# Optimization experiments

Measured on AMD Instinct MI355X. Metric: run time of the kernel, lower is better.

Reference implementation:

```python
import jax, jax.numpy as jnp
import numpy as np

EMB = 1024
HEADS = 16
HD = EMB // HEADS
EPS = 1e-5

def _ln(x, g, b):
    m = jnp.mean(x, axis=-1, keepdims=True)
    v = jnp.mean((x - m) ** 2, axis=-1, keepdims=True)
    return (x - m) * jax.lax.rsqrt(v + EPS) * g + b

def setup_inputs() -> dict:
    key = jax.random.key(0)
    ks = jax.random.split(key, 12)
    s_in = 1.0 / np.sqrt(EMB)
    s_ff = 1.0 / np.sqrt(4 * EMB)
    return {
        "x": jax.random.normal(ks[0], (2, 2048, EMB), jnp.float32),
        "wq": jax.random.uniform(ks[1], (HEADS, EMB, HD), jnp.float32, -s_in, s_in),
        "wk": jax.random.uniform(ks[2], (HEADS, EMB, HD), jnp.float32, -s_in, s_in),
        "wv": jax.random.uniform(ks[3], (HEADS, EMB, HD), jnp.float32, -s_in, s_in),
        "wo": jax.random.uniform(ks[4], (EMB, EMB), jnp.float32, -s_in, s_in),
        "bo": jax.random.uniform(ks[5], (EMB,), jnp.float32, -s_in, s_in),
        "g1": jnp.ones((EMB,), jnp.float32),
        "b1": jnp.zeros((EMB,), jnp.float32),
        "g2": jnp.ones((EMB,), jnp.float32),
        "b2": jnp.zeros((EMB,), jnp.float32),
        "w1": jax.random.uniform(ks[6], (EMB, 4 * EMB), jnp.float32, -s_in, s_in),
        "bf1": jax.random.uniform(ks[7], (4 * EMB,), jnp.float32, -s_in, s_in),
        "w2": jax.random.uniform(ks[8], (4 * EMB, EMB), jnp.float32, -s_ff, s_ff),
        "bf2": jax.random.uniform(ks[9], (EMB,), jnp.float32, -s_ff, s_ff),
    }

def reference(x, wq, wk, wv, wo, bo, g1, b1, g2, b2, w1, bf1, w2, bf2):
    B, T, C = x.shape
    h = _ln(x, g1, b1)
    # all heads batched: [B,H,T,HD]
    q = jnp.einsum('btc,hcd->bhtd', h, wq)
    k = jnp.einsum('btc,hcd->bhtd', h, wk)
    v = jnp.einsum('btc,hcd->bhtd', h, wv)
    # NOTE: original scales by full emb_size C**-0.5, not head_size
    scores = jnp.einsum('bhtd,bhsd->bhts', q, k) * (C ** -0.5)
    causal = jnp.tril(jnp.ones((T, T), bool))
    scores = jnp.where(causal, scores, -jnp.inf)
    w = jax.nn.softmax(scores, axis=-1)
    attn = jnp.einsum('bhts,bhsd->bhtd', w, v)
    attn = attn.transpose(0, 2, 1, 3).reshape(B, T, C)  # concat heads
    x = x + attn @ wo + bo
    h2 = _ln(x, g2, b2)
    ffn = jax.nn.relu(h2 @ w1 + bf1) @ w2 + bf2
    return x + ffn
```

## Files before the change

kernel.cpp:

```cpp
#include <hip/hip_runtime.h>
#include <hip/hip_bf16.h>

typedef __bf16 bf16x8 __attribute__((ext_vector_type(8)));
typedef float f32x4 __attribute__((ext_vector_type(4)));
typedef short s16x8 __attribute__((ext_vector_type(8)));

#define DEV __device__ __forceinline__

DEV float b2f(unsigned short u) {
  unsigned int x = ((unsigned int)u) << 16;
  return __builtin_bit_cast(float, x);
}
DEV unsigned short f2b(float f) {
  unsigned int x = __builtin_bit_cast(unsigned int, f);
  x += 0x7fffu + ((x >> 16) & 1u);
  return (unsigned short)(x >> 16);
}
DEV unsigned int f2b2(float a, float b) {
  float2 t; t.x = a; t.y = b;
  __hip_bfloat162 v = __float22bfloat162_rn(t);
  unsigned int r;
  __builtin_memcpy(&r, &v, 4);
  return r;
}
DEV f32x4 mfma16(bf16x8 a, bf16x8 b, f32x4 c) {
  return __builtin_amdgcn_mfma_f32_16x16x32_bf16(a, b, c, 0, 0, 0);
}
DEV void gl2lds16(const unsigned short* g, unsigned short* l) {
  __builtin_amdgcn_global_load_lds(
      (const __attribute__((address_space(1))) void*)g,
      (__attribute__((address_space(3))) void*)l, 16, 0, 0);
}

__global__ __launch_bounds__(256)
void transpose_k(const float* __restrict__ in, unsigned short* __restrict__ out,
                 int K, int N, long zin, long zout) {
  __shared__ float tile[32][33];
  in  += (size_t)blockIdx.z * zin;
  out += (size_t)blockIdx.z * zout;
  int n0 = blockIdx.x * 32, k0 = blockIdx.y * 32;
  int tx = threadIdx.x, ty = threadIdx.y;
  #pragma unroll
  for (int i = ty; i < 32; i += 8)
    tile[i][tx] = in[(size_t)(k0 + i) * N + n0 + tx];
  __syncthreads();
  #pragma unroll
  for (int i = ty; i < 32; i += 8)
    out[(size_t)(n0 + i) * K + k0 + tx] = f2b(tile[tx][i]);
}

__global__ __launch_bounds__(256)
void transpose_qkv(const float* __restrict__ wq, const float* __restrict__ wk,
                   const float* __restrict__ wv, unsigned short* __restrict__ out) {
  __shared__ float tile[32][33];
  const int z = blockIdx.z;
  const float* in = (z < 16) ? (wq + (size_t)z * 65536)
                  : (z < 32) ? (wk + (size_t)(z - 16) * 65536)
                             : (wv + (size_t)(z - 32) * 65536);
  unsigned short* o = out + (size_t)z * 65536;
  int n0 = blockIdx.x * 32, k0 = blockIdx.y * 32;
  int tx = threadIdx.x, ty = threadIdx.y;
  #pragma unroll
  for (int i = ty; i < 32; i += 8)
    tile[i][tx] = in[(size_t)(k0 + i) * 64 + n0 + tx];
  __syncthreads();
  #pragma unroll
  for (int i = ty; i < 32; i += 8)
    o[(size_t)(n0 + i) * 1024 + k0 + tx] = f2b(tile[tx][i]);
}

__global__ __launch_bounds__(256)
void ln_kernel(const float* __restrict__ x, const float* __restrict__ g,
               const float* __restrict__ b, unsigned short* __restrict__ o) {
  __shared__ float rs[4];
  __shared__ float rq[4];
  int row = blockIdx.x, tid = threadIdx.x;
  const float* xr = x + (size_t)row * 1024;
  float4 raw = ((const float4*)xr)[tid];
  float s = raw.x + raw.y + raw.z + raw.w;
  float q = raw.x*raw.x + raw.y*raw.y + raw.z*raw.z + raw.w*raw.w;
  #pragma unroll
  for (int off = 32; off > 0; off >>= 1) {
    s += __shfl_down(s, off);
    q += __shfl_down(q, off);
  }
  int wave = tid >> 6;
  if ((tid & 63) == 0) { rs[wave] = s; rq[wave] = q; }
  __syncthreads();
  float ts = rs[0] + rs[1] + rs[2] + rs[3];
  float tq = rq[0] + rq[1] + rq[2] + rq[3];
  float mean = ts * (1.0f/1024.0f);
  float var = tq * (1.0f/1024.0f) - mean*mean;
  float rstd = rsqrtf(var + 1e-5f);
  float4 gr = ((const float4*)g)[tid];
  float4 br = ((const float4*)b)[tid];
  float o0 = (raw.x-mean)*rstd*gr.x + br.x;
  float o1 = (raw.y-mean)*rstd*gr.y + br.y;
  float o2 = (raw.z-mean)*rstd*gr.z + br.z;
  float o3 = (raw.w-mean)*rstd*gr.w + br.w;
  uint2 ov;
  ov.x = f2b2(o0, o1);
  ov.y = f2b2(o2, o3);
  ((uint2*)(o + (size_t)row * 1024))[tid] = ov;
}

template<bool RELU, bool BIAS, bool RESID, bool OUTF32, bool VFUSE>
__global__ __launch_bounds__(256)
void gemm_bt(const unsigned short* __restrict__ A, const unsigned short* __restrict__ Bt,
             const float* __restrict__ bias, const float* __restrict__ resid,
             void* __restrict__ Cv, unsigned short* __restrict__ vT, int M, int N, int K) {
  __shared__ unsigned short As[2][128*32];
  __shared__ unsigned short Bs[2][128*32];
  const int tid = threadIdx.x;
  const int lane = tid & 63;
  const int quad = lane >> 4, l16 = lane & 15;
  const int wave = tid >> 6;
  const int m0 = blockIdx.y * 128, n0 = blockIdx.x * 128;
  const int wm = (wave >> 1) * 64, wn = (wave & 1) * 64;

  f32x4 acc[4][4];
  #pragma unroll
  for (int i = 0; i < 4; ++i)
    #pragma unroll
    for (int j = 0; j < 4; ++j) acc[i][j] = (f32x4){0.f, 0.f, 0.f, 0.f};

  const int srow = tid >> 2;
  const int scol = (tid & 3) * 8;
  const unsigned short* Ab = A + (size_t)m0 * K;
  const unsigned short* Bb = Bt + (size_t)n0 * K;

  auto stage = [&](int buf, int k0) {
    gl2lds16(Ab + (size_t)srow * K + k0 + scol,        &As[buf][tid * 8]);
    gl2lds16(Ab + (size_t)(srow + 64) * K + k0 + scol, &As[buf][2048 + tid * 8]);
    gl2lds16(Bb + (size_t)srow * K + k0 + scol,        &Bs[buf][tid * 8]);
    gl2lds16(Bb + (size_t)(srow + 64) * K + k0 + scol, &Bs[buf][2048 + tid * 8]);
  };

  const int niter = K >> 5;
  stage(0, 0);
  __syncthreads();

  for (int it = 0; it < niter; ++it) {
    const int buf = it & 1;
    if (it + 1 < niter) stage(buf ^ 1, (it + 1) * 32);
    bf16x8 af[4], bfr[4];
    #pragma unroll
    for (int i = 0; i < 4; ++i)
      af[i] = __builtin_bit_cast(bf16x8, *(const s16x8*)&As[buf][(wm + i*16 + l16)*32 + quad*8]);
    #pragma unroll
    for (int j = 0; j < 4; ++j)
      bfr[j] = __builtin_bit_cast(bf16x8, *(const s16x8*)&Bs[buf][(wn + j*16 + l16)*32 + quad*8]);
    #pragma unroll
    for (int i = 0; i < 4; ++i)
      #pragma unroll
      for (int j = 0; j < 4; ++j)
        acc[i][j] = mfma16(af[i], bfr[j], acc[i][j]);
    __syncthreads();
  }

  if (VFUSE && n0 >= 2048) {
    #pragma unroll
    for (int i = 0; i < 4; ++i) {
      const int row = m0 + wm + i*16 + quad*4;
      const int b = row >> 11, tloc = row & 2047;
      #pragma unroll
      for (int j = 0; j < 4; ++j) {
        const int col = n0 + wn + j*16 + l16;
        const int h = (col - 2048) >> 6, d = col & 63;
        ushort4 pk;
        pk.x = f2b(acc[i][j][0]);
        pk.y = f2b(acc[i][j][1]);
        pk.z = f2b(acc[i][j][2]);
        pk.w = f2b(acc[i][j][3]);
        *(ushort4*)&vT[((size_t)((b*16 + h)*64 + d))*2048 + tloc] = pk;
      }
    }
    return;
  }

  #pragma unroll
  for (int i = 0; i < 4; ++i) {
    const int row = m0 + wm + i*16 + quad*4;
    #pragma unroll
    for (int j = 0; j < 4; ++j) {
      const int col = n0 + wn + j*16 + l16;
      float bv = 0.f;
      if (BIAS) bv = bias[col];
      #pragma unroll
      for (int r = 0; r < 4; ++r) {
        float v = acc[i][j][r] + bv;
        if (RESID) v += resid[(size_t)(row + r) * N + col];
        if (RELU) v = fmaxf(v, 0.f);
        if (OUTF32) ((float*)Cv)[(size_t)(row + r) * N + col] = v;
        else ((unsigned short*)Cv)[(size_t)(row + r) * N + col] = f2b(v);
      }
    }
  }
}

__global__ __launch_bounds__(256)
void gemm_n1024(const unsigned short* __restrict__ A, const unsigned short* __restrict__ Bt,
                const float* __restrict__ bias, const float* __restrict__ resid,
                float* __restrict__ C, int M, int N, int K) {
  __shared__ unsigned short As[2][64*64];
  __shared__ unsigned short Bs[2][128*64];
  const int tid = threadIdx.x;
  const int lane = tid & 63;
  const int quad = lane >> 4, l16 = lane & 15;
  const int wave = tid >> 6;
  const int id = blockIdx.x;
  const int xcd = id & 7, i2 = id >> 3;
  const int mt = (xcd << 3) | (i2 >> 3);
  const int nt = i2 & 7;
  const int m0 = mt * 64, n0 = nt * 128;
  const int wm = (wave >> 1) * 32, wn = (wave & 1) * 64;

  f32x4 acc[2][4];
  #pragma unroll
  for (int i = 0; i < 2; ++i)
    #pragma unroll
    for (int j = 0; j < 4; ++j) acc[i][j] = (f32x4){0.f, 0.f, 0.f, 0.f};

  const int srow = tid >> 3;
  const int scc  = ((tid & 7) ^ (srow & 7)) * 8;
  const unsigned short* Ab = A + (size_t)m0 * K;
  const unsigned short* Bb = Bt + (size_t)n0 * K;

  auto stage = [&](int buf, int k0) {
    gl2lds16(Ab + (size_t)srow * K + k0 + scc,         &As[buf][tid * 8]);
    gl2lds16(Ab + (size_t)(srow + 32) * K + k0 + scc,  &As[buf][2048 + tid * 8]);
    gl2lds16(Bb + (size_t)srow * K + k0 + scc,         &Bs[buf][tid * 8]);
    gl2lds16(Bb + (size_t)(srow + 32) * K + k0 + scc,  &Bs[buf][2048 + tid * 8]);
    gl2lds16(Bb + (size_t)(srow + 64) * K + k0 + scc,  &Bs[buf][4096 + tid * 8]);
    gl2lds16(Bb + (size_t)(srow + 96) * K + k0 + scc,  &Bs[buf][6144 + tid * 8]);
  };

  const int niter = K >> 6;
  stage(0, 0);
  __syncthreads();

  for (int it = 0; it < niter; ++it) {
    const int buf = it & 1;
    if (it + 1 < niter) stage(buf ^ 1, (it + 1) * 64);
    #pragma unroll
    for (int s = 0; s < 2; ++s) {
      bf16x8 af[2], bfr[4];
      #pragma unroll
      for (int i = 0; i < 2; ++i) {
        const int R = wm + i*16 + l16;
        af[i] = __builtin_bit_cast(bf16x8,
          *(const s16x8*)&As[buf][R*64 + (((s*4 + quad) ^ (R & 7)) * 8)]);
      }
      #pragma unroll
      for (int j = 0; j < 4; ++j) {
        const int R = wn + j*16 + l16;
        bfr[j] = __builtin_bit_cast(bf16x8,
          *(const s16x8*)&Bs[buf][R*64 + (((s*4 + quad) ^ (R & 7)) * 8)]);
      }
      #pragma unroll
      for (int i = 0; i < 2; ++i)
        #pragma unroll
        for (int j = 0; j < 4; ++j)
          acc[i][j] = mfma16(af[i], bfr[j], acc[i][j]);
    }
    __syncthreads();
  }

  #pragma unroll
  for (int i = 0; i < 2; ++i) {
    const int row = m0 + wm + i*16 + quad*4;
    #pragma unroll
    for (int j = 0; j < 4; ++j) {
      const int col = n0 + wn + j*16 + l16;
      const float bv = bias[col];
      #pragma unroll
      for (int r = 0; r < 4; ++r)
        C[(size_t)(row + r) * N + col] = acc[i][j][r] + bv + resid[(size_t)(row + r) * N + col];
    }
  }
}

__global__ __launch_bounds__(256)
void attn_kernel(const unsigned short* __restrict__ qkv,
                 const unsigned short* __restrict__ vT,
                 unsigned short* __restrict__ outc) {
  __shared__ unsigned short Ks[2][64*64];
  __shared__ unsigned short Vs[2][64*64];
  __shared__ unsigned short Ps[4*16*72];
  const int tid = threadIdx.x, lane = tid & 63, wave = tid >> 6;
  const int quad = lane >> 4, l16 = lane & 15;
  const int bh = blockIdx.y, b = bh >> 4, h = bh & 15;
  const int jA = blockIdx.x, jB = 31 - jA;
  const size_t tokbase = (size_t)b * 2048 * 3072;
  const unsigned short* Q  = qkv + tokbase + h * 64;
  const unsigned short* Kg = qkv + tokbase + 1024 + h * 64;
  const unsigned short* Vg = vT + (size_t)bh * 64 * 2048;

  const s16x8 ones_s = {0x3F80, 0x3F80, 0x3F80, 0x3F80, 0x3F80, 0x3F80, 0x3F80, 0x3F80};
  const bf16x8 onesf = __builtin_bit_cast(bf16x8, ones_s);

  bf16x8 qf[2][2];
  #pragma unroll
  for (int t = 0; t < 2; ++t) {
    const int qrow = (t ? jB : jA) * 64 + wave * 16 + l16;
    #pragma unroll
    for (int s = 0; s < 2; ++s) {
      s16x8 raw = *(const s16x8*)(Q + (size_t)qrow * 3072 + s * 32 + quad * 8);
      unsigned short* rp = (unsigned short*)&raw;
      #pragma unroll
      for (int j = 0; j < 8; ++j) rp[j] = f2b(b2f(rp[j]) * 0.03125f);
      qf[t][s] = __builtin_bit_cast(bf16x8, raw);
    }
  }

  f32x4 accO[2][4];
  f32x4 accS[2] = {(f32x4){0.f,0.f,0.f,0.f}, (f32x4){0.f,0.f,0.f,0.f}};
  #pragma unroll
  for (int t = 0; t < 2; ++t)
    #pragma unroll
    for (int i = 0; i < 4; ++i) accO[t][i] = (f32x4){0.f, 0.f, 0.f, 0.f};

  const int r8 = lane >> 3;
  const int cs = (((lane & 7) ^ r8) * 8);

  auto stage = [&](int buf, int kv0) {
    #pragma unroll
    for (int i = 0; i < 2; ++i) {
      int row = wave * 16 + i * 8;
      gl2lds16(Kg + (size_t)(kv0 + row + r8) * 3072 + cs, &Ks[buf][row * 64 + lane * 8]);
      gl2lds16(Vg + (size_t)(row + r8) * 2048 + kv0 + cs, &Vs[buf][row * 64 + lane * 8]);
    }
  };

  const int ntile = jB + 1;
  stage(0, 0);
  __syncthreads();

  for (int it = 0; it < ntile; ++it) {
    const int buf = it & 1;
    if (it + 1 < ntile) stage(buf ^ 1, (it + 1) * 64);

    #pragma unroll
    for (int t = 0; t < 2; ++t) {
      const int jT = t ? jB : jA;
      if (it > jT) continue;
      f32x4 sv[4];
      #pragma unroll
      for (int ni = 0; ni < 4; ++ni) {
        sv[ni] = (f32x4){0.f, 0.f, 0.f, 0.f};
        #pragma unroll
        for (int s = 0; s < 2; ++s) {
          bf16x8 kf = __builtin_bit_cast(bf16x8,
            *(const s16x8*)&Ks[buf][(ni*16 + l16)*64 + (((s*4 + quad) ^ (l16 & 7)) * 8)]);
          sv[ni] = mfma16(qf[t][s], kf, sv[ni]);
        }
      }
      if (it == jT) {
        const int rowg = jT*64 + wave*16 + quad*4;
        const int kv0 = it * 64;
        #pragma unroll
        for (int ni = 0; ni < 4; ++ni) {
          const int colg = kv0 + ni*16 + l16;
          #pragma unroll
          for (int r = 0; r < 4; ++r)
            if (colg > rowg + r) sv[ni][r] = -__builtin_inff();
        }
      }
      #pragma unroll
      for (int ni = 0; ni < 4; ++ni) {
        float p0 = __expf(sv[ni][0]);
        float p1 = __expf(sv[ni][1]);
        float p2 = __expf(sv[ni][2]);
        float p3 = __expf(sv[ni][3]);
        unsigned int u01 = f2b2(p0, p1);
        unsigned int u23 = f2b2(p2, p3);
        const int base = wave*1152 + ni*16 + l16;
        Ps[base + (quad*4 + 0)*72] = (unsigned short)u01;
        Ps[base + (quad*4 + 1)*72] = (unsigned short)(u01 >> 16);
        Ps[base + (quad*4 + 2)*72] = (unsigned short)u23;
        Ps[base + (quad*4 + 3)*72] = (unsigned short)(u23 >> 16);
      }
      __asm__ volatile("s_waitcnt lgkmcnt(0)" ::: "memory");
      #pragma unroll
      for (int s = 0; s < 2; ++s) {
        bf16x8 pf = __builtin_bit_cast(bf16x8,
          *(const s16x8*)&Ps[wave*1152 + l16*72 + s*32 + quad*8]);
        accS[t] = mfma16(pf, onesf, accS[t]);
        #pragma unroll
        for (int ni = 0; ni < 4; ++ni) {
          bf16x8 vf = __builtin_bit_cast(bf16x8,
            *(const s16x8*)&Vs[buf][(ni*16 + l16)*64 + (((s*4 + quad) ^ (l16 & 7)) * 8)]);
          accO[t][ni] = mfma16(pf, vf, accO[t][ni]);
        }
      }
    }
    __syncthreads();
  }

  #pragma unroll
  for (int t = 0; t < 2; ++t) {
    const int rowg = (t ? jB : jA)*64 + wave*16 + quad*4;
    float inv[4];
    #pragma unroll
    for (int r = 0; r < 4; ++r) inv[r] = __builtin_amdgcn_rcpf(accS[t][r]);
    #pragma unroll
    for (int ni = 0; ni < 4; ++ni)
      #pragma unroll
      for (int r = 0; r < 4; ++r)
        outc[(size_t)(b*2048 + rowg + r) * 1024 + h*64 + ni*16 + l16]
          = f2b(accO[t][ni][r] * inv[r]);
  }
}

extern "C" void kernel_launch(void* const* d_in, const int* in_sizes, int n_in,
                              void* d_out, int out_size, void* d_ws, size_t ws_size,
                              hipStream_t stream) {
  (void)in_sizes; (void)n_in; (void)out_size; (void)ws_size;
  const float* x   = (const float*)d_in[0];
  const float* wq  = (const float*)d_in[1];
  const float* wk  = (const float*)d_in[2];
  const float* wv  = (const float*)d_in[3];
  const float* wo  = (const float*)d_in[4];
  const float* bo  = (const float*)d_in[5];
  const float* g1  = (const float*)d_in[6];
  const float* b1  = (const float*)d_in[7];
  const float* g2  = (const float*)d_in[8];
  const float* b2  = (const float*)d_in[9];
  const float* w1  = (const float*)d_in[10];
  const float* bf1 = (const float*)d_in[11];
  const float* w2  = (const float*)d_in[12];
  const float* bf2 = (const float*)d_in[13];
  float* out = (float*)d_out;

  unsigned short* ws    = (unsigned short*)d_ws;
  unsigned short* wqkvt = ws;
  unsigned short* wot   = wqkvt + 3*1024*1024;
  unsigned short* w1t   = wot   + 1024*1024;
  unsigned short* w2t   = w1t   + 4096*1024;
  unsigned short* hbuf  = w2t   + 4096*1024;
  unsigned short* qkvb  = hbuf  + 4096*1024;
  unsigned short* attnb = qkvb  + (size_t)4096*3072;
  float*          x2b   = (float*)(attnb + 4096*1024);
  unsigned short* vTb   = (unsigned short*)x2b;
  unsigned short* midb  = qkvb;

  dim3 tb(32, 8);
  transpose_qkv<<<dim3(2,32,48), tb, 0, stream>>>(wq, wk, wv, wqkvt);
  transpose_k<<<dim3(32,32,1),  tb, 0, stream>>>(wo, wot, 1024, 1024, 0, 0);
  transpose_k<<<dim3(128,32,1), tb, 0, stream>>>(w1, w1t, 1024, 4096, 0, 0);
  transpose_k<<<dim3(32,128,1), tb, 0, stream>>>(w2, w2t, 4096, 1024, 0, 0);

  ln_kernel<<<4096, 256, 0, stream>>>(x, g1, b1, hbuf);
  gemm_bt<false,false,false,false,true><<<dim3(24,32), 256, 0, stream>>>(
      hbuf, wqkvt, nullptr, nullptr, qkvb, vTb, 4096, 3072, 1024);
  attn_kernel<<<dim3(16,32), 256, 0, stream>>>(qkvb, vTb, attnb);
  gemm_n1024<<<512, 256, 0, stream>>>(attnb, wot, bo, x, x2b, 4096, 1024, 1024);
  ln_kernel<<<4096, 256, 0, stream>>>(x2b, g2, b2, hbuf);
  gemm_bt<true,true,false,false,false><<<dim3(32,32), 256, 0, stream>>>(
      hbuf, w1t, bf1, nullptr, midb, nullptr, 4096, 4096, 1024);
  gemm_n1024<<<512, 256, 0, stream>>>(midb, w2t, bf2, x2b, out, 4096, 1024, 4096);
}
```

Baseline: 346.9 us.

## Triple-buffer LDS staging in N=1024 GEMM with vmcnt waits and one barrier

Moves the N=1024 GEMM (output projection and FFN down-projection) from double to triple LDS buffering and prefetches two K-tiles ahead. Explicit s_waitcnt vmcnt counts wait only for the current tile's async global-to-LDS loads, and a single barrier per iteration replaces the trailing __syncthreads. This is meant to hide more global load latency and cut synchronisation. It raises LDS use per block (72KB), which may lower occupancy, and it relies on the vmcnt counts being correct for the async loads.

```diff
diff --git a/kernel.cpp b/kernel.cpp
--- a/kernel.cpp
+++ b/kernel.cpp
@@ -202,8 +202,8 @@
 void gemm_n1024(const unsigned short* __restrict__ A, const unsigned short* __restrict__ Bt,
                 const float* __restrict__ bias, const float* __restrict__ resid,
                 float* __restrict__ C, int M, int N, int K) {
-  __shared__ unsigned short As[2][64*64];
-  __shared__ unsigned short Bs[2][128*64];
+  __shared__ unsigned short As[3][64*64];
+  __shared__ unsigned short Bs[3][128*64];
   const int tid = threadIdx.x;
   const int lane = tid & 63;
   const int quad = lane >> 4, l16 = lane & 15;
@@ -227,21 +227,34 @@
   const unsigned short* Bb = Bt + (size_t)n0 * K;
 
   auto stage = [&](int buf, int k0) {
-    gl2lds16(Ab + (size_t)srow * K + k0 + scc,         &As[buf][tid * 8]);
-    gl2lds16(Ab + (size_t)(srow + 32) * K + k0 + scc,  &As[buf][2048 + tid * 8]);
-    gl2lds16(Bb + (size_t)srow * K + k0 + scc,         &Bs[buf][tid * 8]);
-    gl2lds16(Bb + (size_t)(srow + 32) * K + k0 + scc,  &Bs[buf][2048 + tid * 8]);
-    gl2lds16(Bb + (size_t)(srow + 64) * K + k0 + scc,  &Bs[buf][4096 + tid * 8]);
-    gl2lds16(Bb + (size_t)(srow + 96) * K + k0 + scc,  &Bs[buf][6144 + tid * 8]);
+    unsigned short* Ad = &As[buf][0];
+    unsigned short* Bd = &Bs[buf][0];
+    gl2lds16(Ab + (size_t)srow * K + k0 + scc,         Ad + tid * 8);
+    gl2lds16(Ab + (size_t)(srow + 32) * K + k0 + scc,  Ad + 2048 + tid * 8);
+    gl2lds16(Bb + (size_t)srow * K + k0 + scc,         Bd + tid * 8);
+    gl2lds16(Bb + (size_t)(srow + 32) * K + k0 + scc,  Bd + 2048 + tid * 8);
+    gl2lds16(Bb + (size_t)(srow + 64) * K + k0 + scc,  Bd + 4096 + tid * 8);
+    gl2lds16(Bb + (size_t)(srow + 96) * K + k0 + scc,  Bd + 6144 + tid * 8);
   };
 
   const int niter = K >> 6;
   stage(0, 0);
-  __syncthreads();
-
+  stage(1, 64);
+
+  int bufc = 0;
   for (int it = 0; it < niter; ++it) {
-    const int buf = it & 1;
-    if (it + 1 < niter) stage(buf ^ 1, (it + 1) * 64);
+    if (it + 1 < niter) {
+      asm volatile("s_waitcnt vmcnt(6)" ::: "memory");
+    } else {
+      asm volatile("s_waitcnt vmcnt(0)" ::: "memory");
+    }
+    __builtin_amdgcn_s_barrier();
+    if (it + 2 < niter) {
+      int bufn = bufc + 2; if (bufn >= 3) bufn -= 3;
+      stage(bufn, (it + 2) * 64);
+    }
+    const unsigned short* Ar = &As[bufc][0];
+    const unsigned short* Br = &Bs[bufc][0];
     #pragma unroll
     for (int s = 0; s < 2; ++s) {
       bf16x8 af[2], bfr[4];
@@ -249,13 +262,13 @@
       for (int i = 0; i < 2; ++i) {
         const int R = wm + i*16 + l16;
         af[i] = __builtin_bit_cast(bf16x8,
-          *(const s16x8*)&As[buf][R*64 + (((s*4 + quad) ^ (R & 7)) * 8)]);
+          *(const s16x8*)&Ar[R*64 + (((s*4 + quad) ^ (R & 7)) * 8)]);
       }
       #pragma unroll
       for (int j = 0; j < 4; ++j) {
         const int R = wn + j*16 + l16;
         bfr[j] = __builtin_bit_cast(bf16x8,
-          *(const s16x8*)&Bs[buf][R*64 + (((s*4 + quad) ^ (R & 7)) * 8)]);
+          *(const s16x8*)&Br[R*64 + (((s*4 + quad) ^ (R & 7)) * 8)]);
       }
       #pragma unroll
       for (int i = 0; i < 2; ++i)
@@ -263,7 +276,7 @@
         for (int j = 0; j < 4; ++j)
           acc[i][j] = mfma16(af[i], bfr[j], acc[i][j]);
     }
-    __syncthreads();
+    bufc = (bufc == 2) ? 0 : bufc + 1;
   }
 
   #pragma unroll
```

Result: no change. 345.0 us (-0.5%).

## Replace N=1024 GEMM with 128x128 tile, intra-block split-K kernel

Applied to the files above, without the earlier changes.

The N=1024 output GEMMs (attention projection and FFN down-projection) now use 128x128 tiles with 512 threads instead of 64x128 tiles with 256 threads. The two groups of four waves each handle one half of every 64-wide K slice, and the partial sums are reduced through LDS before the epilogue. Larger tiles improve operand reuse and cut global traffic per FLOP, and the split-K keeps wave count per block high. The cost is fewer blocks (256), an extra LDS reduction and barrier, and dropping the XCD-aware block swizzle.

```diff
diff --git a/kernel.cpp b/kernel.cpp
--- a/kernel.cpp
+++ b/kernel.cpp
@@ -198,26 +198,27 @@
   }
 }
 
-__global__ __launch_bounds__(256)
-void gemm_n1024(const unsigned short* __restrict__ A, const unsigned short* __restrict__ Bt,
-                const float* __restrict__ bias, const float* __restrict__ resid,
-                float* __restrict__ C, int M, int N, int K) {
-  __shared__ unsigned short As[2][64*64];
+__global__ __launch_bounds__(512)
+void gemm_k2(const unsigned short* __restrict__ A, const unsigned short* __restrict__ Bt,
+             const float* __restrict__ bias, const float* __restrict__ resid,
+             float* __restrict__ C, int M, int N, int K) {
+  __shared__ unsigned short As[2][128*64];
   __shared__ unsigned short Bs[2][128*64];
   const int tid = threadIdx.x;
   const int lane = tid & 63;
   const int quad = lane >> 4, l16 = lane & 15;
   const int wave = tid >> 6;
+  const int sub = wave >> 2;
+  const int wq = wave & 3;
+  const int wm = (wq >> 1) * 64, wn = (wq & 1) * 64;
   const int id = blockIdx.x;
-  const int xcd = id & 7, i2 = id >> 3;
-  const int mt = (xcd << 3) | (i2 >> 3);
-  const int nt = i2 & 7;
-  const int m0 = mt * 64, n0 = nt * 128;
-  const int wm = (wave >> 1) * 32, wn = (wave & 1) * 64;
-
-  f32x4 acc[2][4];
-  #pragma unroll
-  for (int i = 0; i < 2; ++i)
+  const int nt = id & 7;
+  const int mt = id >> 3;
+  const int m0 = mt * 128, n0 = nt * 128;
+
+  f32x4 acc[4][4];
+  #pragma unroll
+  for (int i = 0; i < 4; ++i)
     #pragma unroll
     for (int j = 0; j < 4; ++j) acc[i][j] = (f32x4){0.f, 0.f, 0.f, 0.f};
 
@@ -227,12 +228,10 @@
   const unsigned short* Bb = Bt + (size_t)n0 * K;
 
   auto stage = [&](int buf, int k0) {
-    gl2lds16(Ab + (size_t)srow * K + k0 + scc,         &As[buf][tid * 8]);
-    gl2lds16(Ab + (size_t)(srow + 32) * K + k0 + scc,  &As[buf][2048 + tid * 8]);
-    gl2lds16(Bb + (size_t)srow * K + k0 + scc,         &Bs[buf][tid * 8]);
-    gl2lds16(Bb + (size_t)(srow + 32) * K + k0 + scc,  &Bs[buf][2048 + tid * 8]);
-    gl2lds16(Bb + (size_t)(srow + 64) * K + k0 + scc,  &Bs[buf][4096 + tid * 8]);
-    gl2lds16(Bb + (size_t)(srow + 96) * K + k0 + scc,  &Bs[buf][6144 + tid * 8]);
+    gl2lds16(Ab + (size_t)srow * K + k0 + scc,        &As[buf][tid * 8]);
+    gl2lds16(Ab + (size_t)(srow + 64) * K + k0 + scc, &As[buf][4096 + tid * 8]);
+    gl2lds16(Bb + (size_t)srow * K + k0 + scc,        &Bs[buf][tid * 8]);
+    gl2lds16(Bb + (size_t)(srow + 64) * K + k0 + scc, &Bs[buf][4096 + tid * 8]);
   };
 
   const int niter = K >> 6;
@@ -242,40 +241,51 @@
   for (int it = 0; it < niter; ++it) {
     const int buf = it & 1;
     if (it + 1 < niter) stage(buf ^ 1, (it + 1) * 64);
-    #pragma unroll
-    for (int s = 0; s < 2; ++s) {
-      bf16x8 af[2], bfr[4];
-      #pragma unroll
-      for (int i = 0; i < 2; ++i) {
-        const int R = wm + i*16 + l16;
-        af[i] = __builtin_bit_cast(bf16x8,
-          *(const s16x8*)&As[buf][R*64 + (((s*4 + quad) ^ (R & 7)) * 8)]);
-      }
-      #pragma unroll
-      for (int j = 0; j < 4; ++j) {
-        const int R = wn + j*16 + l16;
-        bfr[j] = __builtin_bit_cast(bf16x8,
-          *(const s16x8*)&Bs[buf][R*64 + (((s*4 + quad) ^ (R & 7)) * 8)]);
-      }
-      #pragma unroll
-      for (int i = 0; i < 2; ++i)
-        #pragma unroll
-        for (int j = 0; j < 4; ++j)
-          acc[i][j] = mfma16(af[i], bfr[j], acc[i][j]);
-    }
+    bf16x8 af[4], bfr[4];
+    #pragma unroll
+    for (int i = 0; i < 4; ++i) {
+      const int R = wm + i*16 + l16;
+      af[i] = __builtin_bit_cast(bf16x8,
+        *(const s16x8*)&As[buf][R*64 + (((sub*4 + quad) ^ (R & 7)) * 8)]);
+    }
+    #pragma unroll
+    for (int j = 0; j < 4; ++j) {
+      const int R = wn + j*16 + l16;
+      bfr[j] = __builtin_bit_cast(bf16x8,
+        *(const s16x8*)&Bs[buf][R*64 + (((sub*4 + quad) ^ (R & 7)) * 8)]);
+    }
+    #pragma unroll
+    for (int i = 0; i < 4; ++i)
+      #pragma unroll
+      for (int j = 0; j < 4; ++j)
+        acc[i][j] = mfma16(af[i], bfr[j], acc[i][j]);
     __syncthreads();
   }
 
-  #pragma unroll
-  for (int i = 0; i < 2; ++i) {
+  float* ex = (wq < 2) ? ((float*)&As[0][0] + wq * 4096)
+                       : ((float*)&Bs[0][0] + (wq - 2) * 4096);
+  if (sub == 1) {
+    #pragma unroll
+    for (int i = 0; i < 4; ++i)
+      #pragma unroll
+      for (int j = 0; j < 4; ++j)
+        *(f32x4*)&ex[(i*4 + j)*256 + l16*16 + quad*4] = acc[i][j];
+  }
+  __syncthreads();
+  if (sub == 1) return;
+
+  #pragma unroll
+  for (int i = 0; i < 4; ++i) {
     const int row = m0 + wm + i*16 + quad*4;
     #pragma unroll
     for (int j = 0; j < 4; ++j) {
+      f32x4 oth = *(const f32x4*)&ex[(i*4 + j)*256 + l16*16 + quad*4];
       const int col = n0 + wn + j*16 + l16;
       const float bv = bias[col];
       #pragma unroll
       for (int r = 0; r < 4; ++r)
-        C[(size_t)(row + r) * N + col] = acc[i][j][r] + bv + resid[(size_t)(row + r) * N + col];
+        C[(size_t)(row + r) * N + col] =
+            acc[i][j][r] + oth[r] + bv + resid[(size_t)(row + r) * N + col];
     }
   }
 }
@@ -454,9 +464,9 @@
   gemm_bt<false,false,false,false,true><<<dim3(24,32), 256, 0, stream>>>(
       hbuf, wqkvt, nullptr, nullptr, qkvb, vTb, 4096, 3072, 1024);
   attn_kernel<<<dim3(16,32), 256, 0, stream>>>(qkvb, vTb, attnb);
-  gemm_n1024<<<512, 256, 0, stream>>>(attnb, wot, bo, x, x2b, 4096, 1024, 1024);
+  gemm_k2<<<dim3(256), 512, 0, stream>>>(attnb, wot, bo, x, x2b, 4096, 1024, 1024);
   ln_kernel<<<4096, 256, 0, stream>>>(x2b, g2, b2, hbuf);
   gemm_bt<true,true,false,false,false><<<dim3(32,32), 256, 0, stream>>>(
       hbuf, w1t, bf1, nullptr, midb, nullptr, 4096, 4096, 1024);
-  gemm_n1024<<<512, 256, 0, stream>>>(midb, w2t, bf2, x2b, out, 4096, 1024, 4096);
-}
+  gemm_k2<<<dim3(256), 512, 0, stream>>>(midb, w2t, bf2, x2b, out, 4096, 1024, 4096);
+}
```

Result: slower. 359.9 us (+3.7%).
